# Performance work log

Hardware: AMD Instinct MI355X
Metric: run time of the kernel (lower is better)

## Reference

```python
import jax, jax.numpy as jnp
import numpy as np
import math

EPS = 1e-5

def layernorm(x, g, b):
    mu = jnp.mean(x, axis=-1, keepdims=True)
    var = jnp.var(x, axis=-1, keepdims=True)
    return (x - mu) * jax.lax.rsqrt(var + EPS) * g + b

def setup_inputs() -> dict:
    key = jax.random.key(0)
    ks = jax.random.split(key, 12)
    B, T, E, H = 4, 2048, 128, 8
    D = H * E          # 1024
    F = 4 * D          # 4096
    s = 0.02
    return {
        "X":     jax.random.normal(ks[0], (B, T, E), jnp.float32),
        "ln1_g": jnp.ones((E,), jnp.float32),
        "ln1_b": jnp.zeros((E,), jnp.float32),
        "Wq":    jax.random.normal(ks[1], (H, E, E), jnp.float32) * s,
        "bq":    jax.random.normal(ks[2], (H, E), jnp.float32) * s,
        "Wk":    jax.random.normal(ks[3], (H, E, E), jnp.float32) * s,
        "bk":    jax.random.normal(ks[4], (H, E), jnp.float32) * s,
        "Wv":    jax.random.normal(ks[5], (H, E, E), jnp.float32) * s,
        "bv":    jax.random.normal(ks[6], (H, E), jnp.float32) * s,
        "ln2_g": jnp.ones((D,), jnp.float32),
        "ln2_b": jnp.zeros((D,), jnp.float32),
        "W1":    jax.random.normal(ks[7], (D, F), jnp.float32) * s,
        "b1":    jax.random.normal(ks[8], (F,), jnp.float32) * s,
        "W2":    jax.random.normal(ks[9], (F, E), jnp.float32) * s,
        "b2":    jax.random.normal(ks[10], (E,), jnp.float32) * s,
    }

def reference(X, ln1_g, ln1_b, Wq, bq, Wk, bk, Wv, bv, ln2_g, ln2_b, W1, b1, W2, b2):
    B, T, E = X.shape
    Xn = layernorm(X, ln1_g, ln1_b)                       # [B,T,E]
    # per-head projections, vectorized over heads
    q = jnp.einsum('bte,hef->bhtf', Xn, Wq) + bq[None, :, None, :]
    k = jnp.einsum('bte,hef->bhtf', Xn, Wk) + bk[None, :, None, :]
    v = jnp.einsum('bte,hef->bhtf', Xn, Wv) + bv[None, :, None, :]
    scores = jnp.einsum('bhtf,bhsf->bhts', q, k) / math.sqrt(E)
    # causal mask: positions with s > t set to -inf (triu offset=1)
    t_idx = jnp.arange(T)
    mask = t_idx[None, :] > t_idx[:, None]                # [T,S], True above diag
    scores = jnp.where(mask[None, None], -jnp.inf, scores)
    # NOTE: original code softmaxes over dim = ndim-2, i.e. the QUERY axis
    attn = jax.nn.softmax(scores, axis=-2)
    out = jnp.einsum('bhts,bhsf->bhtf', attn, v)          # [B,H,T,E]
    # concat heads along last dim (head order preserved)
    concat = jnp.transpose(out, (0, 2, 1, 3)).reshape(B, T, -1)  # [B,T,H*E]
    h = layernorm(concat, ln2_g, ln2_b)
    mid = jax.nn.gelu(h @ W1 + b1, approximate=False)
    return mid @ W2 + b2                                   # [B,T,E]
```

## Files before the change

kernel.cpp:

```cpp
#include <hip/hip_runtime.h>
#include <hip/hip_bf16.h>
#include <math.h>

typedef __hip_bfloat16 bf16;
typedef __attribute__((ext_vector_type(8))) short short8;
typedef __attribute__((ext_vector_type(4))) float floatx4;

#define B_ 4
#define T_ 2048
#define E_ 128
#define H_ 8
#define D_ 1024
#define F_ 4096
#define M_ 8192

static __device__ __forceinline__ float b2f(bf16 v){ return __bfloat162float(v); }
static __device__ __forceinline__ bf16  f2b(float v){ return __float2bfloat16(v); }
static __device__ __forceinline__ short f2bs(float v){ bf16 h = __float2bfloat16(v); return *(short*)&h; }

static __device__ __forceinline__ void glds16(const bf16* g, void* l){
  __builtin_amdgcn_global_load_lds((const __attribute__((address_space(1))) void*)g,
                                   (__attribute__((address_space(3))) void*)l, 16, 0, 0);
}

__global__ void detect_dtype_k(const unsigned int* __restrict__ g, int* __restrict__ flag){
  if (threadIdx.x == 0) flag[0] = (g[0] == 0x3F803F80u) ? 1 : 0;
}

__global__ void convert_misc_k(const void* s0, const void* s1, const void* s2, const void* s3,
                               const void* s4, const void* s5, const void* s6, const void* s7,
                               const void* s8,
                               bf16* g1, bf16* b1, bf16* bqkv, bf16* g2, bf16* b2l,
                               bf16* bb1, bf16* bb2, const int* __restrict__ flag){
  int i = blockIdx.x * 256 + threadIdx.x;
  if (i >= 9600) return;
  int fl = flag[0];
  const void* src; bf16* dst; int off;
  if      (i <  128){ src = s0; dst = g1;          off = i;        }
  else if (i <  256){ src = s1; dst = b1;          off = i - 128;  }
  else if (i < 1280){ src = s2; dst = bqkv;        off = i - 256;  }
  else if (i < 2304){ src = s3; dst = bqkv + 1024; off = i - 1280; }
  else if (i < 3328){ src = s4; dst = bqkv + 2048; off = i - 2304; }
  else if (i < 4352){ src = s5; dst = g2;          off = i - 3328; }
  else if (i < 5376){ src = s6; dst = b2l;         off = i - 4352; }
  else if (i < 9472){ src = s7; dst = bb1;         off = i - 5376; }
  else              { src = s8; dst = bb2;         off = i - 9472; }
  dst[off] = fl ? ((const bf16*)src)[off] : f2b(((const float*)src)[off]);
}

__global__ __launch_bounds__(256) void transpose_cvt_k(const void* __restrict__ src, bf16* __restrict__ dst,
                                                       int R, int C, const int* __restrict__ flag){
  __shared__ float tile[32][33];
  int r0 = blockIdx.y * 32, c0 = blockIdx.x * 32;
  int tx = threadIdx.x & 31, ty = threadIdx.x >> 5;
  int fl = flag[0];
  #pragma unroll
  for (int i = 0; i < 32; i += 8){
    size_t idx = (size_t)(r0 + ty + i) * C + c0 + tx;
    tile[ty + i][tx] = fl ? b2f(((const bf16*)src)[idx]) : ((const float*)src)[idx];
  }
  __syncthreads();
  #pragma unroll
  for (int i = 0; i < 32; i += 8){
    dst[(size_t)(c0 + ty + i) * R + r0 + tx] = f2b(tile[tx][ty + i]);
  }
}

__global__ __launch_bounds__(256) void transpose_qkv_k(const void* __restrict__ Wq, const void* __restrict__ Wk,
                                                       const void* __restrict__ Wv, bf16* __restrict__ dst,
                                                       const int* __restrict__ flag){
  __shared__ float tile[32][33];
  int sel = blockIdx.z >> 3, h = blockIdx.z & 7;
  const void* src = (sel == 0) ? Wq : (sel == 1) ? Wk : Wv;
  size_t mo = (size_t)h * E_ * E_;
  bf16* d = dst + (size_t)sel * H_ * E_ * E_ + mo;
  int r0 = blockIdx.y * 32, c0 = blockIdx.x * 32;
  int tx = threadIdx.x & 31, ty = threadIdx.x >> 5;
  int fl = flag[0];
  #pragma unroll
  for (int i = 0; i < 32; i += 8){
    size_t idx = mo + (size_t)(r0 + ty + i) * E_ + c0 + tx;
    tile[ty + i][tx] = fl ? b2f(((const bf16*)src)[idx]) : ((const float*)src)[idx];
  }
  __syncthreads();
  #pragma unroll
  for (int i = 0; i < 32; i += 8){
    d[(size_t)(c0 + ty + i) * E_ + r0 + tx] = f2b(tile[tx][ty + i]);
  }
}

__global__ __launch_bounds__(256) void ln1_k(const void* __restrict__ X, const bf16* __restrict__ g,
                                             const bf16* __restrict__ b, bf16* __restrict__ out,
                                             const int* __restrict__ flag){
  int row = blockIdx.x * 4 + (threadIdx.x >> 6);
  int lane = threadIdx.x & 63;
  float x0, x1;
  if (flag[0]){
    const bf16* xp = (const bf16*)X + (size_t)row * E_;
    x0 = b2f(xp[lane]); x1 = b2f(xp[lane + 64]);
  } else {
    const float* xp = (const float*)X + (size_t)row * E_;
    x0 = xp[lane]; x1 = xp[lane + 64];
  }
  float s  = x0 + x1;
  float s2 = x0 * x0 + x1 * x1;
  #pragma unroll
  for (int o = 32; o > 0; o >>= 1){ s += __shfl_xor(s, o, 64); s2 += __shfl_xor(s2, o, 64); }
  float mu  = s * (1.0f / 128.0f);
  float var = s2 * (1.0f / 128.0f) - mu * mu;
  float rs  = rsqrtf(var + 1e-5f);
  out[(size_t)row * E_ + lane]      = f2b((x0 - mu) * rs * b2f(g[lane])      + b2f(b[lane]));
  out[(size_t)row * E_ + lane + 64] = f2b((x1 - mu) * rs * b2f(g[lane + 64]) + b2f(b[lane + 64]));
}

template<int EPI>
__global__ __launch_bounds__(256, 3) void gemm_coal_k(
    const bf16* __restrict__ A, const bf16* __restrict__ Bt,
    const bf16* __restrict__ bias, void* __restrict__ out,
    int K, const int* __restrict__ flag)
{
  __shared__ __align__(16) short As[2][128][32];
  __shared__ __align__(16) short Bs[2][128][32];
  int tid = threadIdx.x;
  int lane = tid & 63, w = tid >> 6;
  int quad = lane >> 4, l16 = lane & 15;
  int wm = w & 1, wn = w >> 1;
  int m0 = blockIdx.y * 128;
  int n0, nit;
  size_t kstart;
  if (EPI == 3){ n0 = 0; int kc = K >> 3; kstart = (size_t)blockIdx.x * kc; nit = kc >> 5; }
  else         { n0 = blockIdx.x * 128; kstart = 0; nit = K >> 5; }

  int rl = lane >> 2;
  int cg = (lane & 3) ^ ((lane >> 3) & 3);
  int u0 = w * 2, u1 = u0 + 1;
  const bf16* gA0 = A  + (size_t)(m0 + u0 * 16 + rl) * K + kstart + cg * 8;
  const bf16* gA1 = A  + (size_t)(m0 + u1 * 16 + rl) * K + kstart + cg * 8;
  const bf16* gB0 = Bt + (size_t)(n0 + u0 * 16 + rl) * K + kstart + cg * 8;
  const bf16* gB1 = Bt + (size_t)(n0 + u1 * 16 + rl) * K + kstart + cg * 8;

  int offA[4], offB[4];
  #pragma unroll
  for (int i = 0; i < 4; i++){
    int ra = wm * 64 + i * 16 + l16;
    offA[i] = (ra << 6) + ((quad ^ ((ra >> 1) & 3)) << 4);
    int rb = wn * 64 + i * 16 + l16;
    offB[i] = (rb << 6) + ((quad ^ ((rb >> 1) & 3)) << 4);
  }

  glds16(gA0, &As[0][u0 * 16][0]);
  glds16(gA1, &As[0][u1 * 16][0]);
  glds16(gB0, &Bs[0][u0 * 16][0]);
  glds16(gB1, &Bs[0][u1 * 16][0]);
  asm volatile("s_waitcnt vmcnt(0)" ::: "memory");
  __builtin_amdgcn_s_barrier();

  floatx4 acc[4][4];
  #pragma unroll
  for (int i = 0; i < 4; i++)
    #pragma unroll
    for (int j = 0; j < 4; j++) acc[i][j] = (floatx4){0.f, 0.f, 0.f, 0.f};

  #pragma unroll 1
  for (int it = 0; it < nit; it++){
    int buf = it & 1;
    if (it + 1 < nit){
      int ko = (it + 1) << 5;
      glds16(gA0 + ko, &As[buf ^ 1][u0 * 16][0]);
      glds16(gA1 + ko, &As[buf ^ 1][u1 * 16][0]);
      glds16(gB0 + ko, &Bs[buf ^ 1][u0 * 16][0]);
      glds16(gB1 + ko, &Bs[buf ^ 1][u1 * 16][0]);
    }
    const char* bA = (const char*)&As[buf][0][0];
    const char* bB = (const char*)&Bs[buf][0][0];
    short8 af[4], bfr[4];
    #pragma unroll
    for (int i = 0; i < 4; i++) af[i]  = *(const short8*)(bA + offA[i]);
    #pragma unroll
    for (int j = 0; j < 4; j++) bfr[j] = *(const short8*)(bB + offB[j]);
    __builtin_amdgcn_s_setprio(1);
    #pragma unroll
    for (int i = 0; i < 4; i++)
      #pragma unroll
      for (int j = 0; j < 4; j++)
        acc[i][j] = __builtin_amdgcn_mfma_f32_16x16x32_bf16(af[i], bfr[j], acc[i][j], 0, 0, 0);
    __builtin_amdgcn_s_setprio(0);
    if (it + 1 < nit){ asm volatile("s_waitcnt vmcnt(0)" ::: "memory"); }
    asm volatile("s_waitcnt lgkmcnt(0)" ::: "memory");
    __builtin_amdgcn_sched_barrier(0);
    __builtin_amdgcn_s_barrier();
  }

  bf16* po = (EPI == 3) ? (bf16*)out + (size_t)blockIdx.x * M_ * E_ : nullptr;
  #pragma unroll
  for (int i = 0; i < 4; i++){
    #pragma unroll
    for (int j = 0; j < 4; j++){
      int nn = n0 + wn * 64 + j * 16 + l16;
      float bv = (EPI == 3) ? 0.0f : b2f(bias[nn]);
      if (EPI == 0){
        int sel = nn >> 10, h = (nn >> 7) & 7, f = nn & 127;
        size_t SZ = (size_t)B_ * H_ * T_ * E_;
        int mmb = m0 + wm * 64 + i * 16 + quad * 4;
        int b = mmb >> 11, t = mmb & (T_ - 1);
        if (sel < 2){
          #pragma unroll
          for (int r = 0; r < 4; r++)
            ((bf16*)out)[(size_t)sel * SZ + (((size_t)(b * H_ + h) * T_ + t + r) * E_) + f] =
              f2b(acc[i][j][r] + bv);
        } else {
          ushort4 pk;
          #pragma unroll
          for (int r = 0; r < 4; r++) ((short*)&pk)[r] = f2bs(acc[i][j][r] + bv);
          *(ushort4*)((bf16*)out + 2 * SZ + (((size_t)(b * H_ + h) * E_ + f) * T_) + t) = pk;
        }
      } else {
        #pragma unroll
        for (int r = 0; r < 4; r++){
          int mm = m0 + wm * 64 + i * 16 + quad * 4 + r;
          po[(size_t)mm * E_ + nn] = f2b(acc[i][j][r] + bv);
        }
      }
    }
  }
}

__global__ __launch_bounds__(512, 2) void mlp1_swz_k(
    const bf16* __restrict__ A, const bf16* __restrict__ Bt,
    const bf16* __restrict__ bias, bf16* __restrict__ out)
{
  __shared__ __align__(16) short As[4][256][32];
  __shared__ __align__(16) short Bs[4][256][32];
  constexpr int K  = D_;
  constexpr int NK = K / 32;
  constexpr int BUFB = 256 * 32 * 2;

  int tid = threadIdx.x;
  int lane = tid & 63, w = tid >> 6;
  int quad = lane >> 4, l16 = lane & 15;
  int wm = w & 1, wn = w >> 1;
  int orig = blockIdx.y * 16 + blockIdx.x;
  int swz = (orig & 7) * 64 + (orig >> 3);
  int m0 = (swz >> 4) * 256, n0 = (swz & 15) * 256;

  int u0 = w * 2, u1 = u0 + 1;
  int rl = lane >> 2;
  int cg = (lane & 3) ^ ((lane >> 3) & 3);
  const bf16* gA0 = A  + (size_t)(m0 + u0 * 16 + rl) * K + cg * 8;
  const bf16* gA1 = A  + (size_t)(m0 + u1 * 16 + rl) * K + cg * 8;
  const bf16* gB0 = Bt + (size_t)(n0 + u0 * 16 + rl) * K + cg * 8;
  const bf16* gB1 = Bt + (size_t)(n0 + u1 * 16 + rl) * K + cg * 8;

  int offA[2][4], offB[4];
  #pragma unroll
  for (int h = 0; h < 2; h++)
    #pragma unroll
    for (int i = 0; i < 4; i++){
      int ra = wm * 128 + h * 64 + i * 16 + l16;
      offA[h][i] = (ra << 6) + ((quad ^ ((ra >> 1) & 3)) << 4);
    }
  #pragma unroll
  for (int j = 0; j < 4; j++){
    int rb = wn * 64 + j * 16 + l16;
    offB[j] = (rb << 6) + ((quad ^ ((rb >> 1) & 3)) << 4);
  }

  #pragma unroll
  for (int t = 0; t < 3; t++){
    int ko = t * 32;
    glds16(gA0 + ko, &As[t][u0 * 16][0]);
    glds16(gA1 + ko, &As[t][u1 * 16][0]);
    glds16(gB0 + ko, &Bs[t][u0 * 16][0]);
    glds16(gB1 + ko, &Bs[t][u1 * 16][0]);
  }
  asm volatile("s_waitcnt vmcnt(8)" ::: "memory");
  __builtin_amdgcn_s_barrier();

  floatx4 acc[2][4][4];
  #pragma unroll
  for (int h = 0; h < 2; h++)
    #pragma unroll
    for (int i = 0; i < 4; i++)
      #pragma unroll
      for (int j = 0; j < 4; j++) acc[h][i][j] = (floatx4){0.f, 0.f, 0.f, 0.f};

  #pragma unroll 1
  for (int k = 0; k < NK; ++k){
    int bk = k & 3, b3 = (k + 3) & 3;
    const char* baseA = (const char*)As + bk * BUFB;
    const char* baseB = (const char*)Bs + bk * BUFB;
    short8 bf8[4], a2[2][4];
    #pragma unroll
    for (int j = 0; j < 4; j++) bf8[j]   = *(const short8*)(baseB + offB[j]);
    #pragma unroll
    for (int i = 0; i < 4; i++) a2[0][i] = *(const short8*)(baseA + offA[0][i]);
    #pragma unroll
    for (int i = 0; i < 4; i++) a2[1][i] = *(const short8*)(baseA + offA[1][i]);
    if (k + 3 < NK){
      int ko = (k + 3) * 32;
      glds16(gA0 + ko, &As[b3][u0 * 16][0]);
      glds16(gA1 + ko, &As[b3][u1 * 16][0]);
      glds16(gB0 + ko, &Bs[b3][u0 * 16][0]);
      glds16(gB1 + ko, &Bs[b3][u1 * 16][0]);
    }
    __builtin_amdgcn_s_setprio(1);
    #pragma unroll
    for (int h = 0; h < 2; h++)
      #pragma unroll
      for (int i = 0; i < 4; i++)
        #pragma unroll
        for (int j = 0; j < 4; j++)
          acc[h][i][j] = __builtin_amdgcn_mfma_f32_16x16x32_bf16(a2[h][i], bf8[j], acc[h][i][j], 0, 0, 0);
    __builtin_amdgcn_s_setprio(0);
    if (k < NK - 3)       { asm volatile("s_waitcnt vmcnt(8)" ::: "memory"); }
    else if (k == NK - 3) { asm volatile("s_waitcnt vmcnt(4)" ::: "memory"); }
    else if (k == NK - 2) { asm volatile("s_waitcnt vmcnt(0)" ::: "memory"); }
    asm volatile("s_waitcnt lgkmcnt(0)" ::: "memory");
    __builtin_amdgcn_sched_barrier(0);
    __builtin_amdgcn_s_barrier();
  }

  #pragma unroll
  for (int h = 0; h < 2; h++){
    #pragma unroll
    for (int i = 0; i < 4; i++){
      #pragma unroll
      for (int j = 0; j < 4; j++){
        int nn = n0 + wn * 64 + j * 16 + l16;
        float bv = b2f(bias[nn]);
        #pragma unroll
        for (int r = 0; r < 4; r++){
          int mm = m0 + wm * 128 + h * 64 + i * 16 + quad * 4 + r;
          float v = acc[h][i][j][r] + bv;
          float e = __expf(1.5957691216057308f * v * (1.0f + 0.044715f * v * v));
          out[(size_t)mm * F_ + nn] = f2b(v - v / (1.0f + e));
        }
      }
    }
  }
}

__global__ __launch_bounds__(256) void mlp2_fin_k(const bf16* __restrict__ P, const bf16* __restrict__ bias,
                                                  void* __restrict__ out, const int* __restrict__ flag){
  int i = blockIdx.x * 256 + threadIdx.x;
  const size_t S = (size_t)M_ * E_;
  float v = b2f(bias[i & (E_ - 1)]);
  #pragma unroll
  for (int k = 0; k < 8; k++) v += b2f(P[i + k * S]);
  if (flag[0]) ((bf16*)out)[i] = f2b(v);
  else         ((float*)out)[i] = v;
}

__global__ __launch_bounds__(256, 2) void colstats_k(const bf16* __restrict__ Q, const bf16* __restrict__ K,
                                                     float* __restrict__ IL){
  __shared__ __align__(16) short Qs[2][128][128];
  __shared__ float lcol[64];
  const float scale = 0.0883883476483184f;
  int tid = threadIdx.x;
  int lane = tid & 63, w = tid >> 6;
  int quad = lane >> 4, l16 = lane & 15;
  int x = blockIdx.x;
  int bh = x & 31, sblk = x >> 5;
  int s0 = sblk * 64;

  short8 bk[4][4];
  #pragma unroll
  for (int j = 0; j < 4; j++)
    #pragma unroll
    for (int kb = 0; kb < 4; kb++)
      bk[j][kb] = *(const short8*)(K + ((size_t)bh * T_ + s0 + j * 16 + l16) * E_ + kb * 32 + quad * 8);

  if (tid < 64) lcol[tid] = 0.0f;

  int t0s = (s0 / 128) * 128;
  int nit = (T_ - t0s) >> 7;

  int srow = lane >> 4, schunk = lane & 15;
  #pragma unroll
  for (int t2 = 0; t2 < 8; t2++){
    int u = w * 8 + t2;
    int r = u * 4 + srow;
    const bf16* ga = Q + ((size_t)bh * T_ + t0s + r) * E_ + (schunk ^ (r & 7)) * 8;
    glds16(ga, &Qs[0][u * 4][0]);
  }
  __syncthreads();

  float part[4] = {0.f, 0.f, 0.f, 0.f};
  for (int it = 0; it < nit; it++){
    int buf = it & 1;
    if (it + 1 < nit){
      int nb = buf ^ 1;
      int t1 = t0s + ((it + 1) << 7);
      #pragma unroll
      for (int t2 = 0; t2 < 8; t2++){
        int u = w * 8 + t2;
        int r = u * 4 + srow;
        const bf16* ga = Q + ((size_t)bh * T_ + t1 + r) * E_ + (schunk ^ (r & 7)) * 8;
        glds16(ga, &Qs[nb][u * 4][0]);
      }
    }
    floatx4 acc[2][4];
    #pragma unroll
    for (int i = 0; i < 2; i++)
      #pragma unroll
      for (int j = 0; j < 4; j++) acc[i][j] = (floatx4){0.f, 0.f, 0.f, 0.f};
    #pragma unroll
    for (int kb = 0; kb < 4; kb++){
      short8 af[2];
      #pragma unroll
      for (int i = 0; i < 2; i++){
        int row = w * 32 + i * 16 + l16;
        af[i] = *(const short8*)((const char*)&Qs[buf][0][0] + (row << 8)
                                 + ((((kb << 2) + quad) ^ (l16 & 7)) << 4));
      }
      #pragma unroll
      for (int i = 0; i < 2; i++)
        #pragma unroll
        for (int j = 0; j < 4; j++)
          acc[i][j] = __builtin_amdgcn_mfma_f32_16x16x32_bf16(af[i], bk[j][kb], acc[i][j], 0, 0, 0);
    }
    int t0 = t0s + (it << 7);
    bool dtile = (it == 0);
    #pragma unroll
    for (int i = 0; i < 2; i++)
      #pragma unroll
      for (int j = 0; j < 4; j++)
        #pragma unroll
        for (int r = 0; r < 4; r++){
          float e = __expf(acc[i][j][r] * scale);
          if (dtile){
            int t = t0 + w * 32 + i * 16 + quad * 4 + r;
            int s = s0 + j * 16 + l16;
            if (t < s) e = 0.0f;
          }
          part[j] += e;
        }
    __syncthreads();
  }
  #pragma unroll
  for (int j = 0; j < 4; j++){
    part[j] += __shfl_xor(part[j], 16, 64);
    part[j] += __shfl_xor(part[j], 32, 64);
  }
  if (quad == 0){
    #pragma unroll
    for (int j = 0; j < 4; j++) atomicAdd(&lcol[j * 16 + l16], part[j]);
  }
  __syncthreads();
  if (tid < 64) IL[(size_t)bh * T_ + s0 + tid] = 1.0f / lcol[tid];
}

__global__ __launch_bounds__(256, 2) void attnout_k(const bf16* __restrict__ Q, const bf16* __restrict__ K,
                                                    const bf16* __restrict__ VT, const float* __restrict__ IL,
                                                    bf16* __restrict__ CC){
  __shared__ __align__(16) short Ks[64][128];
  __shared__ __align__(16) short Vs[128][64];
  __shared__ __align__(16) short Ps[128][72];
  const float scale = 0.0883883476483184f;
  int tid = threadIdx.x;
  int lane = tid & 63, w = tid >> 6;
  int quad = lane >> 4, l16 = lane & 15;
  int x = blockIdx.x;
  int bh = x & 31, tblk = x >> 5;
  int t0 = tblk * 128;
  int b = bh >> 3, h = bh & 7;

  short8 qf[2][4];
  #pragma unroll
  for (int i = 0; i < 2; i++)
    #pragma unroll
    for (int kb = 0; kb < 4; kb++)
      qf[i][kb] = *(const short8*)(Q + ((size_t)bh * T_ + t0 + w * 32 + i * 16 + l16) * E_ + kb * 32 + quad * 8);

  floatx4 O[2][8];
  #pragma unroll
  for (int i = 0; i < 2; i++)
    #pragma unroll
    for (int n = 0; n < 8; n++) O[i][n] = (floatx4){0.f, 0.f, 0.f, 0.f};

  int ksrow = lane >> 4, kschunk = lane & 15;
  int vsrow = lane >> 3, vschunk = lane & 7;

  for (int s0 = 0; s0 < t0 + 128; s0 += 64){
    __syncthreads();
    #pragma unroll
    for (int t = 0; t < 4; t++){
      int u = w * 4 + t;
      int r = u * 4 + ksrow;
      const bf16* ga = K + ((size_t)bh * T_ + s0 + r) * E_ + ((kschunk ^ (r & 7)) * 8);
      glds16(ga, &Ks[u * 4][0]);
    }
    #pragma unroll
    for (int t = 0; t < 4; t++){
      int u = w * 4 + t;
      int e = u * 8 + vsrow;
      const bf16* ga = VT + ((size_t)bh * E_ + e) * T_ + s0 + ((vschunk ^ (e & 7)) * 8);
      glds16(ga, &Vs[u * 8][0]);
    }
    __syncthreads();
    floatx4 acc[2][4];
    #pragma unroll
    for (int i = 0; i < 2; i++)
      #pragma unroll
      for (int j = 0; j < 4; j++) acc[i][j] = (floatx4){0.f, 0.f, 0.f, 0.f};
    __builtin_amdgcn_s_setprio(1);
    #pragma unroll
    for (int kb = 0; kb < 4; kb++){
      short8 bfr[4];
      #pragma unroll
      for (int j = 0; j < 4; j++)
        bfr[j] = *(const short8*)&Ks[j * 16 + l16][(((kb << 2) + quad) ^ (l16 & 7)) * 8];
      #pragma unroll
      for (int i = 0; i < 2; i++)
        #pragma unroll
        for (int j = 0; j < 4; j++)
          acc[i][j] = __builtin_amdgcn_mfma_f32_16x16x32_bf16(qf[i][kb], bfr[j], acc[i][j], 0, 0, 0);
    }
    __builtin_amdgcn_s_setprio(0);
    float il[4];
    #pragma unroll
    for (int j = 0; j < 4; j++) il[j] = IL[(size_t)bh * T_ + s0 + j * 16 + l16];
    bool dtile = (s0 + 63 > t0);
    #pragma unroll
    for (int i = 0; i < 2; i++)
      #pragma unroll
      for (int j = 0; j < 4; j++)
        #pragma unroll
        for (int r = 0; r < 4; r++){
          float p = __expf(acc[i][j][r] * scale) * il[j];
          int trow = w * 32 + i * 16 + quad * 4 + r;
          if (dtile){
            int t = t0 + trow, s = s0 + j * 16 + l16;
            if (t < s) p = 0.0f;
          }
          Ps[trow][j * 16 + l16] = f2bs(p);
        }
    __syncthreads();
    __builtin_amdgcn_s_setprio(1);
    #pragma unroll
    for (int kb2 = 0; kb2 < 2; kb2++){
      short8 pa[2], vb[8];
      #pragma unroll
      for (int i = 0; i < 2; i++) pa[i] = *(const short8*)&Ps[w * 32 + i * 16 + l16][kb2 * 32 + quad * 8];
      #pragma unroll
      for (int n = 0; n < 8; n++)
        vb[n] = *(const short8*)&Vs[n * 16 + l16][(((kb2 << 2) + quad) ^ (l16 & 7)) * 8];
      #pragma unroll
      for (int i = 0; i < 2; i++)
        #pragma unroll
        for (int n = 0; n < 8; n++)
          O[i][n] = __builtin_amdgcn_mfma_f32_16x16x32_bf16(pa[i], vb[n], O[i][n], 0, 0, 0);
    }
    __builtin_amdgcn_s_setprio(0);
  }
  #pragma unroll
  for (int i = 0; i < 2; i++)
    #pragma unroll
    for (int n = 0; n < 8; n++)
      #pragma unroll
      for (int r = 0; r < 4; r++){
        int t = t0 + w * 32 + i * 16 + quad * 4 + r;
        int e = n * 16 + l16;
        CC[((size_t)(b * T_ + t)) * D_ + h * E_ + e] = f2b(O[i][n][r]);
      }
}

__global__ __launch_bounds__(256) void ln2_k(const bf16* __restrict__ in, const bf16* __restrict__ g,
                                             const bf16* __restrict__ bta, bf16* __restrict__ out){
  __shared__ float wsum[4], wsum2[4];
  int row = blockIdx.x, tid = threadIdx.x;
  const bf16* xp = in + (size_t)row * D_;
  float x[4]; float s = 0.0f, s2 = 0.0f;
  #pragma unroll
  for (int i = 0; i < 4; i++){ x[i] = b2f(xp[tid + i * 256]); s += x[i]; s2 += x[i] * x[i]; }
  #pragma unroll
  for (int o = 32; o > 0; o >>= 1){ s += __shfl_xor(s, o, 64); s2 += __shfl_xor(s2, o, 64); }
  int wid = tid >> 6;
  if ((tid & 63) == 0){ wsum[wid] = s; wsum2[wid] = s2; }
  __syncthreads();
  s  = wsum[0] + wsum[1] + wsum[2] + wsum[3];
  s2 = wsum2[0] + wsum2[1] + wsum2[2] + wsum2[3];
  float mu  = s * (1.0f / 1024.0f);
  float var = s2 * (1.0f / 1024.0f) - mu * mu;
  float rs  = rsqrtf(var + 1e-5f);
  #pragma unroll
  for (int i = 0; i < 4; i++){
    int c = tid + i * 256;
    out[(size_t)row * D_ + c] = f2b((x[i] - mu) * rs * b2f(g[c]) + b2f(bta[c]));
  }
}

static constexpr size_t A256(size_t x){ return (x + 255) & ~(size_t)255; }

extern "C" void kernel_launch(void* const* d_in, const int* in_sizes, int n_in,
                              void* d_out, int out_size, void* d_ws, size_t ws_size,
                              hipStream_t stream){
  (void)in_sizes; (void)n_in; (void)out_size; (void)ws_size;
  char* ws = (char*)d_ws;

  constexpr size_t o_flag  = 0;
  constexpr size_t o_g1    = 256;
  constexpr size_t o_b1    = A256(o_g1    + (size_t)E_ * 2);
  constexpr size_t o_WqkvT = A256(o_b1    + (size_t)E_ * 2);
  constexpr size_t o_bqkv  = A256(o_WqkvT + (size_t)3 * H_ * E_ * E_ * 2);
  constexpr size_t o_g2    = A256(o_bqkv  + (size_t)3 * H_ * E_ * 2);
  constexpr size_t o_b2l   = A256(o_g2    + (size_t)D_ * 2);
  constexpr size_t o_W1T   = A256(o_b2l   + (size_t)D_ * 2);
  constexpr size_t o_bb1   = A256(o_W1T   + (size_t)D_ * F_ * 2);
  constexpr size_t o_W2T   = A256(o_bb1   + (size_t)F_ * 2);
  constexpr size_t o_bb2   = A256(o_W2T   + (size_t)F_ * E_ * 2);
  constexpr size_t o_xn    = A256(o_bb2   + (size_t)E_ * 2);
  constexpr size_t o_q     = A256(o_xn    + (size_t)M_ * E_ * 2);
  constexpr size_t o_k     = o_q + (size_t)B_ * H_ * T_ * E_ * 2;
  constexpr size_t o_vt    = o_k + (size_t)B_ * H_ * T_ * E_ * 2;
  constexpr size_t o_il    = A256(o_vt + (size_t)B_ * H_ * T_ * E_ * 2);
  constexpr size_t o_cc    = A256(o_il + (size_t)B_ * H_ * T_ * 4);
  constexpr size_t o_h2    = A256(o_cc + (size_t)M_ * D_ * 2);
  constexpr size_t o_mid   = o_q;
  constexpr size_t o_part  = o_h2;
  static_assert(o_mid + (size_t)M_ * F_ * 2 <= o_h2, "mid overlaps live h2 buffer");
  static_assert((size_t)8 * M_ * E_ * 2 <= (size_t)M_ * D_ * 2, "partials exceed h2 region");

  int*  flag  = (int*)(ws + o_flag);
  bf16* g1    = (bf16*)(ws + o_g1);
  bf16* b1p   = (bf16*)(ws + o_b1);
  bf16* WqkvT = (bf16*)(ws + o_WqkvT);
  bf16* bqkv  = (bf16*)(ws + o_bqkv);
  bf16* g2    = (bf16*)(ws + o_g2);
  bf16* b2l   = (bf16*)(ws + o_b2l);
  bf16* W1T   = (bf16*)(ws + o_W1T);
  bf16* bb1   = (bf16*)(ws + o_bb1);
  bf16* W2T   = (bf16*)(ws + o_W2T);
  bf16* bb2   = (bf16*)(ws + o_bb2);
  bf16* xn    = (bf16*)(ws + o_xn);
  bf16* Qb    = (bf16*)(ws + o_q);
  bf16* Kb    = (bf16*)(ws + o_k);
  bf16* VTb   = (bf16*)(ws + o_vt);
  float* ILp  = (float*)(ws + o_il);
  bf16* ccp   = (bf16*)(ws + o_cc);
  bf16* h2p   = (bf16*)(ws + o_h2);
  bf16* midp  = (bf16*)(ws + o_mid);
  bf16* part  = (bf16*)(ws + o_part);

  detect_dtype_k<<<1, 64, 0, stream>>>((const unsigned int*)d_in[1], flag);

  convert_misc_k<<<38, 256, 0, stream>>>(d_in[1], d_in[2], d_in[4], d_in[6], d_in[8],
                                         d_in[9], d_in[10], d_in[12], d_in[14],
                                         g1, b1p, bqkv, g2, b2l, bb1, bb2, flag);

  transpose_qkv_k<<<dim3(4, 4, 24), 256, 0, stream>>>(d_in[3], d_in[5], d_in[7], WqkvT, flag);
  transpose_cvt_k<<<dim3(F_ / 32, D_ / 32), 256, 0, stream>>>(d_in[11], W1T, D_, F_, flag);
  transpose_cvt_k<<<dim3(E_ / 32, F_ / 32), 256, 0, stream>>>(d_in[13], W2T, F_, E_, flag);

  ln1_k<<<M_ / 4, 256, 0, stream>>>(d_in[0], g1, b1p, xn, flag);

  gemm_coal_k<0><<<dim3(3 * D_ / 128, M_ / 128), 256, 0, stream>>>(xn, WqkvT, bqkv, Qb, E_, flag);

  colstats_k<<<1024, 256, 0, stream>>>(Qb, Kb, ILp);
  attnout_k<<<512, 256, 0, stream>>>(Qb, Kb, VTb, ILp, ccp);

  ln2_k<<<M_, 256, 0, stream>>>(ccp, g2, b2l, h2p);

  mlp1_swz_k<<<dim3(F_ / 256, M_ / 256), 512, 0, stream>>>(h2p, W1T, bb1, midp);
  gemm_coal_k<3><<<dim3(8, M_ / 128), 256, 0, stream>>>(midp, W2T, bb2, part, F_, flag);
  mlp2_fin_k<<<M_ * E_ / 256, 256, 0, stream>>>(part, bb2, d_out, flag);
}
```

Before: 346.1 us.

## Replace dedicated 256x256 MLP1 GEMM with generic 128-tile GEMM plus GELU epilogue

Removes the specialized 512-thread, 256x256-tile, 4-stage pipelined MLP1 kernel and instead runs the first MLP matmul through the generic gemm_coal_k template with a new GELU epilogue variant. The generic kernel uses 128x128 tiles with 256 threads, giving four times as many blocks. This trades the larger tile's data reuse and tuned software pipelining for simpler code and possibly better occupancy or load balance.

```diff
diff --git a/kernel.cpp b/kernel.cpp
--- a/kernel.cpp
+++ b/kernel.cpp
@@ -214,126 +214,19 @@
           for (int r = 0; r < 4; r++) ((short*)&pk)[r] = f2bs(acc[i][j][r] + bv);
           *(ushort4*)((bf16*)out + 2 * SZ + (((size_t)(b * H_ + h) * E_ + f) * T_) + t) = pk;
         }
+      } else if (EPI == 1){
+        #pragma unroll
+        for (int r = 0; r < 4; r++){
+          int mm = m0 + wm * 64 + i * 16 + quad * 4 + r;
+          float v = acc[i][j][r] + bv;
+          float e = __expf(1.5957691216057308f * v * (1.0f + 0.044715f * v * v));
+          ((bf16*)out)[(size_t)mm * F_ + nn] = f2b(v - v / (1.0f + e));
+        }
       } else {
         #pragma unroll
         for (int r = 0; r < 4; r++){
           int mm = m0 + wm * 64 + i * 16 + quad * 4 + r;
           po[(size_t)mm * E_ + nn] = f2b(acc[i][j][r] + bv);
-        }
-      }
-    }
-  }
-}
-
-__global__ __launch_bounds__(512, 2) void mlp1_swz_k(
-    const bf16* __restrict__ A, const bf16* __restrict__ Bt,
-    const bf16* __restrict__ bias, bf16* __restrict__ out)
-{
-  __shared__ __align__(16) short As[4][256][32];
-  __shared__ __align__(16) short Bs[4][256][32];
-  constexpr int K  = D_;
-  constexpr int NK = K / 32;
-  constexpr int BUFB = 256 * 32 * 2;
-
-  int tid = threadIdx.x;
-  int lane = tid & 63, w = tid >> 6;
-  int quad = lane >> 4, l16 = lane & 15;
-  int wm = w & 1, wn = w >> 1;
-  int orig = blockIdx.y * 16 + blockIdx.x;
-  int swz = (orig & 7) * 64 + (orig >> 3);
-  int m0 = (swz >> 4) * 256, n0 = (swz & 15) * 256;
-
-  int u0 = w * 2, u1 = u0 + 1;
-  int rl = lane >> 2;
-  int cg = (lane & 3) ^ ((lane >> 3) & 3);
-  const bf16* gA0 = A  + (size_t)(m0 + u0 * 16 + rl) * K + cg * 8;
-  const bf16* gA1 = A  + (size_t)(m0 + u1 * 16 + rl) * K + cg * 8;
-  const bf16* gB0 = Bt + (size_t)(n0 + u0 * 16 + rl) * K + cg * 8;
-  const bf16* gB1 = Bt + (size_t)(n0 + u1 * 16 + rl) * K + cg * 8;
-
-  int offA[2][4], offB[4];
-  #pragma unroll
-  for (int h = 0; h < 2; h++)
-    #pragma unroll
-    for (int i = 0; i < 4; i++){
-      int ra = wm * 128 + h * 64 + i * 16 + l16;
-      offA[h][i] = (ra << 6) + ((quad ^ ((ra >> 1) & 3)) << 4);
-    }
-  #pragma unroll
-  for (int j = 0; j < 4; j++){
-    int rb = wn * 64 + j * 16 + l16;
-    offB[j] = (rb << 6) + ((quad ^ ((rb >> 1) & 3)) << 4);
-  }
-
-  #pragma unroll
-  for (int t = 0; t < 3; t++){
-    int ko = t * 32;
-    glds16(gA0 + ko, &As[t][u0 * 16][0]);
-    glds16(gA1 + ko, &As[t][u1 * 16][0]);
-    glds16(gB0 + ko, &Bs[t][u0 * 16][0]);
-    glds16(gB1 + ko, &Bs[t][u1 * 16][0]);
-  }
-  asm volatile("s_waitcnt vmcnt(8)" ::: "memory");
-  __builtin_amdgcn_s_barrier();
-
-  floatx4 acc[2][4][4];
-  #pragma unroll
-  for (int h = 0; h < 2; h++)
-    #pragma unroll
-    for (int i = 0; i < 4; i++)
-      #pragma unroll
-      for (int j = 0; j < 4; j++) acc[h][i][j] = (floatx4){0.f, 0.f, 0.f, 0.f};
-
-  #pragma unroll 1
-  for (int k = 0; k < NK; ++k){
-    int bk = k & 3, b3 = (k + 3) & 3;
-    const char* baseA = (const char*)As + bk * BUFB;
-    const char* baseB = (const char*)Bs + bk * BUFB;
-    short8 bf8[4], a2[2][4];
-    #pragma unroll
-    for (int j = 0; j < 4; j++) bf8[j]   = *(const short8*)(baseB + offB[j]);
-    #pragma unroll
-    for (int i = 0; i < 4; i++) a2[0][i] = *(const short8*)(baseA + offA[0][i]);
-    #pragma unroll
-    for (int i = 0; i < 4; i++) a2[1][i] = *(const short8*)(baseA + offA[1][i]);
-    if (k + 3 < NK){
-      int ko = (k + 3) * 32;
-      glds16(gA0 + ko, &As[b3][u0 * 16][0]);
-      glds16(gA1 + ko, &As[b3][u1 * 16][0]);
-      glds16(gB0 + ko, &Bs[b3][u0 * 16][0]);
-      glds16(gB1 + ko, &Bs[b3][u1 * 16][0]);
-    }
-    __builtin_amdgcn_s_setprio(1);
-    #pragma unroll
-    for (int h = 0; h < 2; h++)
-      #pragma unroll
-      for (int i = 0; i < 4; i++)
-        #pragma unroll
-        for (int j = 0; j < 4; j++)
-          acc[h][i][j] = __builtin_amdgcn_mfma_f32_16x16x32_bf16(a2[h][i], bf8[j], acc[h][i][j], 0, 0, 0);
-    __builtin_amdgcn_s_setprio(0);
-    if (k < NK - 3)       { asm volatile("s_waitcnt vmcnt(8)" ::: "memory"); }
-    else if (k == NK - 3) { asm volatile("s_waitcnt vmcnt(4)" ::: "memory"); }
-    else if (k == NK - 2) { asm volatile("s_waitcnt vmcnt(0)" ::: "memory"); }
-    asm volatile("s_waitcnt lgkmcnt(0)" ::: "memory");
-    __builtin_amdgcn_sched_barrier(0);
-    __builtin_amdgcn_s_barrier();
-  }
-
-  #pragma unroll
-  for (int h = 0; h < 2; h++){
-    #pragma unroll
-    for (int i = 0; i < 4; i++){
-      #pragma unroll
-      for (int j = 0; j < 4; j++){
-        int nn = n0 + wn * 64 + j * 16 + l16;
-        float bv = b2f(bias[nn]);
-        #pragma unroll
-        for (int r = 0; r < 4; r++){
-          int mm = m0 + wm * 128 + h * 64 + i * 16 + quad * 4 + r;
-          float v = acc[h][i][j][r] + bv;
-          float e = __expf(1.5957691216057308f * v * (1.0f + 0.044715f * v * v));
-          out[(size_t)mm * F_ + nn] = f2b(v - v / (1.0f + e));
         }
       }
     }
@@ -661,7 +554,7 @@
 
   ln2_k<<<M_, 256, 0, stream>>>(ccp, g2, b2l, h2p);
 
-  mlp1_swz_k<<<dim3(F_ / 256, M_ / 256), 512, 0, stream>>>(h2p, W1T, bb1, midp);
+  gemm_coal_k<1><<<dim3(F_ / 128, M_ / 128), 256, 0, stream>>>(h2p, W1T, bb1, midp, D_, flag);
   gemm_coal_k<3><<<dim3(8, M_ / 128), 256, 0, stream>>>(midp, W2T, bb2, part, F_, flag);
   mlp2_fin_k<<<M_ * E_ / 256, 256, 0, stream>>>(part, bb2, d_out, flag);
 }
```

New measurement: 353.4 us. 2.1% more time.
